# Kernel tuning notes

Measured on AMD Instinct MI355X. Metric: run time of the kernel, lower is better.

## Reference

```python
import jax, jax.numpy as jnp
import numpy as np

B, N, DIN, DOUT = 32, 1024, 256, 256


def setup_inputs() -> dict:
    key = jax.random.key(0)
    ks = jax.random.split(key, 7)
    s = 1.0 / np.sqrt(DIN)
    return {
        "x": jax.random.normal(ks[0], (B, N, DIN), dtype=jnp.float32),
        "Wq": jax.random.uniform(ks[1], (DOUT, DIN), minval=-s, maxval=s, dtype=jnp.float32),
        "bq": jax.random.uniform(ks[2], (DOUT,), minval=-s, maxval=s, dtype=jnp.float32),
        "Wk": jax.random.uniform(ks[3], (DOUT, DIN), minval=-s, maxval=s, dtype=jnp.float32),
        "bk": jax.random.uniform(ks[4], (DOUT,), minval=-s, maxval=s, dtype=jnp.float32),
        "Wv": jax.random.uniform(ks[5], (DOUT, DIN), minval=-s, maxval=s, dtype=jnp.float32),
        "bv": jax.random.uniform(ks[6], (DOUT,), minval=-s, maxval=s, dtype=jnp.float32),
    }


def reference(x, Wq, bq, Wk, bk, Wv, bv):
    # q, k, v: (B, N, Dout)
    q = jnp.einsum("bnd,od->bno", x, Wq) + bq
    k = jnp.einsum("bnd,od->bno", x, Wk) + bk
    v = jnp.einsum("bnd,od->bno", x, Wv) + bv
    # logits: (B, N, N) = q @ k^T per batch
    logits = jnp.einsum("bnd,bmd->bnm", q, k)
    # NOTE: softmax over the BATCH dim (axis=0), as in the original module
    attn = jax.nn.softmax(logits, axis=0)
    out = jnp.einsum("bnm,bmd->bnd", attn, v)  # (B, N, Dout)
    return out
```

## Files before the change

### kernel.cpp

```cpp
#include <hip/hip_runtime.h>

typedef __bf16 bf16x8 __attribute__((ext_vector_type(8)));
typedef __bf16 bf16x4 __attribute__((ext_vector_type(4)));
typedef float  f32x4  __attribute__((ext_vector_type(4)));

#define BK 64

__device__ __forceinline__ void g2l16(const void* g, void* l) {
    __builtin_amdgcn_global_load_lds((const __attribute__((address_space(1))) void*)g,
                                     (__attribute__((address_space(3))) void*)l, 16, 0, 0);
}


__global__ __launch_bounds__(256)
void gemm_proj(const __bf16* __restrict__ A, const __bf16* __restrict__ Wb,
               __bf16* __restrict__ qkv, const float* __restrict__ bpack)
{
    __shared__ __align__(16) __bf16 smem[3 * 12288];

    const int tid  = threadIdx.x;
    const int w    = tid >> 6;
    const int lane = tid & 63;
    const int quad = lane >> 4;
    const int l16  = lane & 15;
    const int wm   = w & 1;
    const int wn   = w >> 1;

    const int m0 = blockIdx.x * 128;
    const int n0 = blockIdx.y * 64;
    const int z  = blockIdx.z;

    const __bf16* Bb   = Wb + (size_t)z * 131072;
    const float*  bias = bpack + z * 256;

    const int srow = (w << 3) + (lane >> 3);
    const int scol = ((lane & 7) ^ (lane >> 3)) << 3;

    const __bf16* Ag = A  + (size_t)(m0 + srow) * 256 + scol;
    const __bf16* Bg = Bb + (size_t)(n0 + srow) * 256 + scol;

    f32x4 acc[4][2] = {};

    auto STAGE = [&](int buf, int k0) {
        char* base = (char*)smem + buf * 24576;
        #pragma unroll
        for (int c = 0; c < 4; c++)
            g2l16(Ag + (size_t)(c * 32) * 256 + k0, base + w * 1024 + c * 4096);
        #pragma unroll
        for (int c = 0; c < 2; c++)
            g2l16(Bg + (size_t)(c * 32) * 256 + k0, base + 16384 + w * 1024 + c * 4096);
    };

    STAGE(0, 0);
    STAGE(1, 64);

    for (int t = 0; t < 4; t++) {
        if (t < 3) asm volatile("s_waitcnt vmcnt(6)" ::: "memory");
        else       asm volatile("s_waitcnt vmcnt(0)" ::: "memory");
        __builtin_amdgcn_sched_barrier(0);
        __builtin_amdgcn_s_barrier();

        if (t < 2) STAGE((t + 2) % 3, (t + 2) * BK);

        const __bf16* As = smem + (t % 3) * 12288;
        const __bf16* Bs = As + 8192;
        #pragma unroll
        for (int kk = 0; kk < BK; kk += 32) {
            const int ub = kk >> 3;
            bf16x8 a[4], b[2];
            #pragma unroll
            for (int mt = 0; mt < 4; mt++) {
                const int row = wm * 64 + mt * 16 + l16;
                const int cp  = ((quad + ub) ^ (row & 7)) << 3;
                a[mt] = *(const bf16x8*)&As[row * BK + cp];
            }
            #pragma unroll
            for (int nt = 0; nt < 2; nt++) {
                const int row = wn * 32 + nt * 16 + l16;
                const int cp  = ((quad + ub) ^ (row & 7)) << 3;
                b[nt] = *(const bf16x8*)&Bs[row * BK + cp];
            }
            #pragma unroll
            for (int mt = 0; mt < 4; mt++)
                #pragma unroll
                for (int nt = 0; nt < 2; nt++)
                    acc[mt][nt] = __builtin_amdgcn_mfma_f32_16x16x32_bf16(
                        a[mt], b[nt], acc[mt][nt], 0, 0, 0);
        }
    }

    __syncthreads();
    if (z < 2) {
        #pragma unroll
        for (int mt = 0; mt < 4; mt++) {
            const int rl = wm * 64 + mt * 16 + quad * 4;
            #pragma unroll
            for (int nt = 0; nt < 2; nt++) {
                const int cl = wn * 32 + nt * 16 + l16;
                const float bn = bias[n0 + cl];
                #pragma unroll
                for (int r = 0; r < 4; r++) {
                    const int row = rl + r;
                    smem[row * 64 + ((((cl >> 3) ^ (row & 7)) << 3) | (cl & 7))] =
                        (__bf16)(acc[mt][nt][r] + bn);
                }
            }
        }
        __syncthreads();
        __bf16* C = qkv + (size_t)z * 8388608;
        #pragma unroll
        for (int i = 0; i < 4; i++) {
            const int c   = tid + i * 256;
            const int row = c >> 3, u = c & 7;
            *(bf16x8*)&C[(size_t)(m0 + row) * 256 + n0 + u * 8] =
                *(const bf16x8*)&smem[row * 64 + ((u ^ (row & 7)) << 3)];
        }
    } else {
        #pragma unroll
        for (int mt = 0; mt < 4; mt++) {
            const int ml = wm * 64 + mt * 16 + quad * 4;
            #pragma unroll
            for (int nt = 0; nt < 2; nt++) {
                const int dl = wn * 32 + nt * 16 + l16;
                const float bn = bias[n0 + dl];
                bf16x4 pk;
                #pragma unroll
                for (int r = 0; r < 4; r++) pk[r] = (__bf16)(acc[mt][nt][r] + bn);
                *(bf16x4*)&smem[dl * 128 + ((((ml >> 3) ^ (dl & 7)) << 3) | (ml & 7))] = pk;
            }
        }
        __syncthreads();
        __bf16* C = qkv + 2 * 8388608;
        const int bidx = m0 >> 10, mbase = m0 & 1023;
        #pragma unroll
        for (int i = 0; i < 4; i++) {
            const int c  = tid + i * 256;
            const int dl = c >> 4, u = c & 15;
            *(bf16x8*)&C[(size_t)bidx * 262144 + (size_t)(n0 + dl) * 1024 + mbase + u * 8] =
                *(const bf16x8*)&smem[dl * 128 + ((u ^ (dl & 7)) << 3)];
        }
    }
}

__global__ __launch_bounds__(256, 1)
void gemm_logits(const __bf16* __restrict__ Q, const __bf16* __restrict__ Km,
                 __bf16* __restrict__ E)
{
    __shared__ __align__(16) __bf16 smem[2 * 24576];

    const int tid  = threadIdx.x;
    const int w    = tid >> 6;
    const int lane = tid & 63;
    const int quad = lane >> 4;
    const int l16  = lane & 15;
    const int wm   = w & 1;
    const int wn   = w >> 1;

    const int id = blockIdx.x;
    const int x  = id & 7, g = id >> 3;
    const int z  = x + ((g >> 5) << 3);
    const int gt = g & 31;
    const int m0 = (gt & 7) * 128;
    const int n0 = (gt >> 3) * 256;

    const __bf16* Ab = Q  + (size_t)z * 262144;
    const __bf16* Bb = Km + (size_t)z * 262144;

    const int srow = (w << 3) + (lane >> 3);
    const int scol = ((lane & 7) ^ (lane >> 3)) << 3;

    const __bf16* Ag = Ab + (size_t)(m0 + srow) * 256 + scol;
    const __bf16* Bg = Bb + (size_t)(n0 + srow) * 256 + scol;

    f32x4 acc[4][8] = {};

    auto STAGE = [&](int buf, int k0) {
        char* base = (char*)smem + buf * 49152;
        #pragma unroll
        for (int c = 0; c < 4; c++)
            g2l16(Ag + (size_t)(c * 32) * 256 + k0, base + w * 1024 + c * 4096);
        #pragma unroll
        for (int c = 0; c < 8; c++)
            g2l16(Bg + (size_t)(c * 32) * 256 + k0, base + 16384 + w * 1024 + c * 4096);
    };

    STAGE(0, 0);
    STAGE(1, 64);

    for (int t = 0; t < 4; t++) {
        if (t < 3) asm volatile("s_waitcnt vmcnt(12)" ::: "memory");
        else       asm volatile("s_waitcnt vmcnt(0)"  ::: "memory");
        __builtin_amdgcn_sched_barrier(0);
        __builtin_amdgcn_s_barrier();

        const __bf16* As = smem + (t & 1) * 24576;
        const __bf16* Bs = As + 8192;
        #pragma unroll
        for (int kk = 0; kk < BK; kk += 32) {
            const int ub = kk >> 3;
            bf16x8 a[4], b[8];
            #pragma unroll
            for (int mt = 0; mt < 4; mt++) {
                const int row = wm * 64 + mt * 16 + l16;
                const int cp  = ((quad + ub) ^ (row & 7)) << 3;
                a[mt] = *(const bf16x8*)&As[row * BK + cp];
            }
            #pragma unroll
            for (int nt = 0; nt < 8; nt++) {
                const int row = wn * 128 + nt * 16 + l16;
                const int cp  = ((quad + ub) ^ (row & 7)) << 3;
                b[nt] = *(const bf16x8*)&Bs[row * BK + cp];
            }
            #pragma unroll
            for (int mt = 0; mt < 4; mt++)
                #pragma unroll
                for (int nt = 0; nt < 8; nt++)
                    acc[mt][nt] = __builtin_amdgcn_mfma_f32_16x16x32_bf16(
                        a[mt], b[nt], acc[mt][nt], 0, 0, 0);
        }

        __builtin_amdgcn_s_barrier();

        if (t < 2) STAGE(t & 1, (t + 2) * BK);
    }

    __syncthreads();
    #pragma unroll
    for (int mt = 0; mt < 4; mt++) {
        const int rl = wm * 64 + mt * 16 + quad * 4;
        #pragma unroll
        for (int nt = 0; nt < 8; nt++) {
            const int cl = wn * 128 + nt * 16 + l16;
            #pragma unroll
            for (int r = 0; r < 4; r++) {
                const int row = rl + r;
                smem[row * 256 + ((((cl >> 3) ^ (row & 7)) << 3) | (cl & 7))] =
                    (__bf16)__expf(acc[mt][nt][r]);
            }
        }
    }
    __syncthreads();
    __bf16* C = E + (size_t)z * 1048576;
    #pragma unroll
    for (int i = 0; i < 16; i++) {
        const int c   = tid + i * 256;
        const int row = c >> 5, u = c & 31;
        *(bf16x8*)&C[(size_t)(m0 + row) * 1024 + n0 + u * 8] =
            *(const bf16x8*)&smem[row * 256 + ((u ^ (row & 7)) << 3)];
    }
}

__global__ __launch_bounds__(256)
void sum_rcp(const __bf16* __restrict__ E, __bf16* __restrict__ rcpS)
{
    const size_t p = (size_t)blockIdx.x * 256 + threadIdx.x;
    const bf16x8* E8 = (const bf16x8*)E;
    float s[8] = {0.f, 0.f, 0.f, 0.f, 0.f, 0.f, 0.f, 0.f};
    #pragma unroll
    for (int b = 0; b < 32; b++) {
        const bf16x8 e = E8[(size_t)b * 131072 + p];
        #pragma unroll
        for (int j = 0; j < 8; j++) s[j] += (float)e[j];
    }
    bf16x8 o;
    #pragma unroll
    for (int j = 0; j < 8; j++) o[j] = (__bf16)__builtin_amdgcn_rcpf(s[j]);
    ((bf16x8*)rcpS)[p] = o;
}

__global__ __launch_bounds__(256, 1)
void gemm_pv(const __bf16* __restrict__ En, const __bf16* __restrict__ rcpS,
             const __bf16* __restrict__ vT, float* __restrict__ out)
{
    __shared__ __align__(16) __bf16 smem[2 * 24576];

    const int tid  = threadIdx.x;
    const int w    = tid >> 6;
    const int lane = tid & 63;
    const int quad = lane >> 4;
    const int l16  = lane & 15;
    const int wm   = w & 1;
    const int wn   = w >> 1;

    const int id = blockIdx.x;
    const int x  = id & 7, g = id >> 3;
    const int z  = x + ((g & 3) << 3);
    const int m0 = (g >> 2) * 128;

    const __bf16* Eb = En + (size_t)z * 1048576;
    const __bf16* Vb = vT + (size_t)z * 262144;
    float*        Ob = out + (size_t)z * 262144;

    const int srow = (w << 3) + (lane >> 3);
    const int scol = ((lane & 7) ^ (lane >> 3)) << 3;

    const __bf16* Ag = Eb   + (size_t)(m0 + srow) * 1024 + scol;
    const __bf16* Rg = rcpS + (size_t)(m0 + srow) * 1024 + scol;
    const __bf16* Bg = Vb   + (size_t)srow * 1024 + scol;

    f32x4 acc[4][8] = {};
    bf16x8 e[4], rs[4];

    auto LOAD_ER = [&](int k0) {
        #pragma unroll
        for (int c = 0; c < 4; c++) {
            e[c]  = *(const bf16x8*)(Ag + (size_t)(c * 32) * 1024 + k0);
            rs[c] = *(const bf16x8*)(Rg + (size_t)(c * 32) * 1024 + k0);
        }
    };
    auto G2L_B = [&](int buf, int k0) {
        char* base = (char*)smem + buf * 49152 + 16384;
        #pragma unroll
        for (int c = 0; c < 8; c++)
            g2l16(Bg + (size_t)(c * 32) * 1024 + k0, base + w * 1024 + c * 4096);
    };
    auto WRITE_A = [&](int buf) {
        char* base = (char*)smem + buf * 49152;
        #pragma unroll
        for (int c = 0; c < 4; c++) {
            bf16x8 o;
            #pragma unroll
            for (int j = 0; j < 8; j++)
                o[j] = (__bf16)((float)e[c][j] * (float)rs[c][j]);
            *(bf16x8*)(base + w * 1024 + lane * 16 + c * 4096) = o;
        }
    };

    LOAD_ER(0);
    G2L_B(0, 0);
    asm volatile("s_waitcnt vmcnt(8)" ::: "memory");
    __builtin_amdgcn_sched_barrier(0);
    WRITE_A(0);
    LOAD_ER(64);
    G2L_B(1, 64);

    for (int t = 0; t < 16; t++) {
        if (t < 15) asm volatile("s_waitcnt vmcnt(16)" ::: "memory");
        else        asm volatile("s_waitcnt vmcnt(0)"  ::: "memory");
        __builtin_amdgcn_sched_barrier(0);
        asm volatile("s_waitcnt lgkmcnt(0)" ::: "memory");
        __builtin_amdgcn_sched_barrier(0);
        __builtin_amdgcn_s_barrier();

        const __bf16* As = smem + (t & 1) * 24576;
        const __bf16* Bs = As + 8192;
        #pragma unroll
        for (int kk = 0; kk < BK; kk += 32) {
            const int ub = kk >> 3;
            bf16x8 a[4], b[8];
            #pragma unroll
            for (int mt = 0; mt < 4; mt++) {
                const int row = wm * 64 + mt * 16 + l16;
                const int cp  = ((quad + ub) ^ (row & 7)) << 3;
                a[mt] = *(const bf16x8*)&As[row * BK + cp];
            }
            #pragma unroll
            for (int nt = 0; nt < 8; nt++) {
                const int row = wn * 128 + nt * 16 + l16;
                const int cp  = ((quad + ub) ^ (row & 7)) << 3;
                b[nt] = *(const bf16x8*)&Bs[row * BK + cp];
            }
            #pragma unroll
            for (int mt = 0; mt < 4; mt++)
                #pragma unroll
                for (int nt = 0; nt < 8; nt++)
                    acc[mt][nt] = __builtin_amdgcn_mfma_f32_16x16x32_bf16(
                        a[mt], b[nt], acc[mt][nt], 0, 0, 0);
        }

        __builtin_amdgcn_s_barrier();

        if (t < 15) {
            asm volatile("s_waitcnt vmcnt(8)" ::: "memory");
            __builtin_amdgcn_sched_barrier(0);
            WRITE_A((t + 1) & 1);
            if (t < 14) {
                LOAD_ER((t + 2) * BK);
                G2L_B(t & 1, (t + 2) * BK);
            }
        }
    }

    #pragma unroll
    for (int mt = 0; mt < 4; mt++) {
        const int mb = m0 + wm * 64 + mt * 16 + quad * 4;
        #pragma unroll
        for (int nt = 0; nt < 8; nt++) {
            const int n = wn * 128 + nt * 16 + l16;
            #pragma unroll
            for (int r = 0; r < 4; r++)
                Ob[(size_t)(mb + r) * 256 + n] = acc[mt][nt][r];
        }
    }
}

__global__ __launch_bounds__(256)
void cvt_all(const float* __restrict__ x,
             const float* __restrict__ Wq, const float* __restrict__ Wk,
             const float* __restrict__ Wv,
             const float* __restrict__ bq, const float* __restrict__ bk,
             const float* __restrict__ bv,
             __bf16* __restrict__ xb, __bf16* __restrict__ Wqb,
             float* __restrict__ bpack)
{
    const int i = blockIdx.x * 256 + threadIdx.x;
    if (i < 1073152) {
        const float* s; __bf16* d; int off;
        if (i < 1048576)      { s = x;  d = xb;            off = i; }
        else if (i < 1056768) { s = Wq; d = Wqb;           off = i - 1048576; }
        else if (i < 1064960) { s = Wk; d = Wqb + 131072;  off = i - 1056768; }
        else                  { s = Wv; d = Wqb + 262144;  off = i - 1064960; }
        const float4* s4 = (const float4*)s;
        const float4 f0 = s4[off * 2], f1 = s4[off * 2 + 1];
        bf16x8 o;
        o[0] = (__bf16)f0.x; o[1] = (__bf16)f0.y; o[2] = (__bf16)f0.z; o[3] = (__bf16)f0.w;
        o[4] = (__bf16)f1.x; o[5] = (__bf16)f1.y; o[6] = (__bf16)f1.z; o[7] = (__bf16)f1.w;
        ((bf16x8*)d)[off] = o;
    } else if (i < 1073344) {
        const int j = i - 1073152;
        const int sel = j >> 6, jj = j & 63;
        const float* s = sel == 0 ? bq : (sel == 1 ? bk : bv);
        ((float4*)bpack)[j] = ((const float4*)s)[jj];
    }
}

extern "C" void kernel_launch(void* const* d_in, const int* in_sizes, int n_in,
                              void* d_out, int out_size, void* d_ws, size_t ws_size,
                              hipStream_t stream)
{
    const float* x  = (const float*)d_in[0];
    const float* Wq = (const float*)d_in[1];
    const float* bq = (const float*)d_in[2];
    const float* Wk = (const float*)d_in[3];
    const float* bk = (const float*)d_in[4];
    const float* Wv = (const float*)d_in[5];
    const float* bv = (const float*)d_in[6];
    float* out = (float*)d_out;

    char* ws = (char*)d_ws;
    __bf16* rcpS = (__bf16*)ws;
    __bf16* xb   = (__bf16*)(ws + (2u  << 20));
    __bf16* qkv  = (__bf16*)(ws + (18u << 20));
    __bf16* E    = (__bf16*)(ws + (66u << 20));
    __bf16* Wqb  = (__bf16*)(ws + (130u << 20));
    float*  bpack = (float*)(ws + (130u << 20) + (1u << 20));

    cvt_all<<<4194, 256, 0, stream>>>(x, Wq, Wk, Wv, bq, bk, bv, xb, Wqb, bpack);

    gemm_proj<<<dim3(256, 4, 3), 256, 0, stream>>>(xb, Wqb, qkv, bpack);

    gemm_logits<<<1024, 256, 0, stream>>>(qkv, qkv + 8388608, E);

    sum_rcp<<<512, 256, 0, stream>>>(E, rcpS);

    gemm_pv<<<256, 256, 0, stream>>>(E, rcpS, qkv + 2 * 8388608, out);
}
```

Before: 188.6 us.

## Make gemm_logits blocks persistent over full rows with register-resident Q fragments

Each gemm_logits block now owns a 128-row Q strip and walks all four 256-column K tiles, instead of one 128x256 output tile per block. The Q strip is loaded into LDS once and held in registers across tiles, while K tiles are streamed through a double buffer that keeps prefetching during each tile's exp/store epilogue. The grid shrinks from 1024 to 256 blocks, one per CU, which removes repeated Q loads and the block tail across waves. The cost is heavy register pressure from the resident A fragments plus accumulators, 128KB of LDS, and less parallelism to hide latency.

```diff
diff --git a/kernel.cpp b/kernel.cpp
--- a/kernel.cpp
+++ b/kernel.cpp
@@ -146,7 +146,7 @@
 void gemm_logits(const __bf16* __restrict__ Q, const __bf16* __restrict__ Km,
                  __bf16* __restrict__ E)
 {
-    __shared__ __align__(16) __bf16 smem[2 * 24576];
+    __shared__ __align__(16) __bf16 smem[65536];
 
     const int tid  = threadIdx.x;
     const int w    = tid >> 6;
@@ -158,10 +158,8 @@
 
     const int id = blockIdx.x;
     const int x  = id & 7, g = id >> 3;
-    const int z  = x + ((g >> 5) << 3);
-    const int gt = g & 31;
-    const int m0 = (gt & 7) * 128;
-    const int n0 = (gt >> 3) * 256;
+    const int z  = x + ((g & 3) << 3);
+    const int m0 = (g >> 2) * 128;
 
     const __bf16* Ab = Q  + (size_t)z * 262144;
     const __bf16* Bb = Km + (size_t)z * 262144;
@@ -170,83 +168,112 @@
     const int scol = ((lane & 7) ^ (lane >> 3)) << 3;
 
     const __bf16* Ag = Ab + (size_t)(m0 + srow) * 256 + scol;
-    const __bf16* Bg = Bb + (size_t)(n0 + srow) * 256 + scol;
-
-    f32x4 acc[4][8] = {};
-
-    auto STAGE = [&](int buf, int k0) {
-        char* base = (char*)smem + buf * 49152;
+    const __bf16* Bg = Bb + (size_t)srow * 256 + scol;
+
+    #pragma unroll
+    for (int kc = 0; kc < 4; kc++)
         #pragma unroll
         for (int c = 0; c < 4; c++)
-            g2l16(Ag + (size_t)(c * 32) * 256 + k0, base + w * 1024 + c * 4096);
+            g2l16(Ag + (size_t)(c * 32) * 256 + kc * 64,
+                  (char*)smem + kc * 16384 + w * 1024 + c * 4096);
+
+    auto STAGE_B = [&](int buf, int tile, int k0) {
+        char* base = (char*)smem + 65536 + buf * 32768;
         #pragma unroll
         for (int c = 0; c < 8; c++)
-            g2l16(Bg + (size_t)(c * 32) * 256 + k0, base + 16384 + w * 1024 + c * 4096);
+            g2l16(Bg + (size_t)(tile * 256 + c * 32) * 256 + k0,
+                  base + w * 1024 + c * 4096);
     };
-
-    STAGE(0, 0);
-    STAGE(1, 64);
-
-    for (int t = 0; t < 4; t++) {
-        if (t < 3) asm volatile("s_waitcnt vmcnt(12)" ::: "memory");
-        else       asm volatile("s_waitcnt vmcnt(0)"  ::: "memory");
+    STAGE_B(0, 0, 0);
+    STAGE_B(1, 0, 64);
+
+    asm volatile("s_waitcnt vmcnt(16)" ::: "memory");
+    __builtin_amdgcn_sched_barrier(0);
+    __builtin_amdgcn_s_barrier();
+
+    bf16x8 afr[4][8];
+    #pragma unroll
+    for (int mt = 0; mt < 4; mt++) {
+        const int row = wm * 64 + mt * 16 + l16;
+        #pragma unroll
+        for (int kc = 0; kc < 4; kc++)
+            #pragma unroll
+            for (int h = 0; h < 2; h++)
+                afr[mt][kc * 2 + h] =
+                    *(const bf16x8*)&smem[kc * 8192 + row * 64 +
+                                          ((((quad + h * 4)) ^ (row & 7)) << 3)];
+    }
+
+    f32x4 acc[4][8];
+    __bf16* C = E + (size_t)z * 1048576;
+
+    #pragma unroll
+    for (int tile = 0; tile < 4; tile++) {
+        #pragma unroll
+        for (int mt = 0; mt < 4; mt++)
+            #pragma unroll
+            for (int nt = 0; nt < 8; nt++)
+                acc[mt][nt] = f32x4{0.f, 0.f, 0.f, 0.f};
+
+        #pragma unroll
+        for (int j = 0; j < 4; j++) {
+            const int i = tile * 4 + j;
+            if (tile == 0)          asm volatile("s_waitcnt vmcnt(8)"  ::: "memory");
+            else if (j < 2)         asm volatile("s_waitcnt vmcnt(24)" ::: "memory");
+            else if (i == 15)       asm volatile("s_waitcnt vmcnt(0)"  ::: "memory");
+            else                    asm volatile("s_waitcnt vmcnt(8)"  ::: "memory");
+            __builtin_amdgcn_sched_barrier(0);
+            __builtin_amdgcn_s_barrier();
+
+            const __bf16* Bs = smem + 32768 + (i & 1) * 16384;
+            #pragma unroll
+            for (int h = 0; h < 2; h++) {
+                bf16x8 b[8];
+                #pragma unroll
+                for (int nt = 0; nt < 8; nt++) {
+                    const int row = wn * 128 + nt * 16 + l16;
+                    const int cp  = ((quad + h * 4) ^ (row & 7)) << 3;
+                    b[nt] = *(const bf16x8*)&Bs[row * BK + cp];
+                }
+                #pragma unroll
+                for (int mt = 0; mt < 4; mt++)
+                    #pragma unroll
+                    for (int nt = 0; nt < 8; nt++)
+                        acc[mt][nt] = __builtin_amdgcn_mfma_f32_16x16x32_bf16(
+                            afr[mt][j * 2 + h], b[nt], acc[mt][nt], 0, 0, 0);
+            }
+            __builtin_amdgcn_s_barrier();
+
+            if (i + 2 <= 15)
+                STAGE_B(i & 1, (i + 2) >> 2, ((i + 2) & 3) * 64);
+        }
+
+        #pragma unroll
+        for (int mt = 0; mt < 4; mt++) {
+            const int rl = wm * 64 + mt * 16 + quad * 4;
+            #pragma unroll
+            for (int nt = 0; nt < 8; nt++) {
+                const int cl = wn * 128 + nt * 16 + l16;
+                #pragma unroll
+                for (int r = 0; r < 4; r++) {
+                    const int row = rl + r;
+                    smem[row * 256 + ((((cl >> 3) ^ (row & 7)) << 3) | (cl & 7))] =
+                        (__bf16)__expf(acc[mt][nt][r]);
+                }
+            }
+        }
+        asm volatile("s_waitcnt lgkmcnt(0)" ::: "memory");
         __builtin_amdgcn_sched_barrier(0);
         __builtin_amdgcn_s_barrier();
 
-        const __bf16* As = smem + (t & 1) * 24576;
-        const __bf16* Bs = As + 8192;
-        #pragma unroll
-        for (int kk = 0; kk < BK; kk += 32) {
-            const int ub = kk >> 3;
-            bf16x8 a[4], b[8];
-            #pragma unroll
-            for (int mt = 0; mt < 4; mt++) {
-                const int row = wm * 64 + mt * 16 + l16;
-                const int cp  = ((quad + ub) ^ (row & 7)) << 3;
-                a[mt] = *(const bf16x8*)&As[row * BK + cp];
-            }
-            #pragma unroll
-            for (int nt = 0; nt < 8; nt++) {
-                const int row = wn * 128 + nt * 16 + l16;
-                const int cp  = ((quad + ub) ^ (row & 7)) << 3;
-                b[nt] = *(const bf16x8*)&Bs[row * BK + cp];
-            }
-            #pragma unroll
-            for (int mt = 0; mt < 4; mt++)
-                #pragma unroll
-                for (int nt = 0; nt < 8; nt++)
-                    acc[mt][nt] = __builtin_amdgcn_mfma_f32_16x16x32_bf16(
-                        a[mt], b[nt], acc[mt][nt], 0, 0, 0);
-        }
-
-        __builtin_amdgcn_s_barrier();
-
-        if (t < 2) STAGE(t & 1, (t + 2) * BK);
-    }
-
-    __syncthreads();
-    #pragma unroll
-    for (int mt = 0; mt < 4; mt++) {
-        const int rl = wm * 64 + mt * 16 + quad * 4;
-        #pragma unroll
-        for (int nt = 0; nt < 8; nt++) {
-            const int cl = wn * 128 + nt * 16 + l16;
-            #pragma unroll
-            for (int r = 0; r < 4; r++) {
-                const int row = rl + r;
-                smem[row * 256 + ((((cl >> 3) ^ (row & 7)) << 3) | (cl & 7))] =
-                    (__bf16)__expf(acc[mt][nt][r]);
-            }
-        }
-    }
-    __syncthreads();
-    __bf16* C = E + (size_t)z * 1048576;
-    #pragma unroll
-    for (int i = 0; i < 16; i++) {
-        const int c   = tid + i * 256;
-        const int row = c >> 5, u = c & 31;
-        *(bf16x8*)&C[(size_t)(m0 + row) * 1024 + n0 + u * 8] =
-            *(const bf16x8*)&smem[row * 256 + ((u ^ (row & 7)) << 3)];
+        const int n0 = tile * 256;
+        #pragma unroll
+        for (int ii = 0; ii < 16; ii++) {
+            const int c   = tid + ii * 256;
+            const int row = c >> 5, u = c & 31;
+            *(bf16x8*)&C[(size_t)(m0 + row) * 1024 + n0 + u * 8] =
+                *(const bf16x8*)&smem[row * 256 + ((u ^ (row & 7)) << 3)];
+        }
     }
 }
 
@@ -449,7 +476,7 @@
 
     gemm_proj<<<dim3(256, 4, 3), 256, 0, stream>>>(xb, Wqb, qkv, bpack);
 
-    gemm_logits<<<1024, 256, 0, stream>>>(qkv, qkv + 8388608, E);
+    gemm_logits<<<256, 256, 0, stream>>>(qkv, qkv + 8388608, E);
 
     sum_rcp<<<512, 256, 0, stream>>>(E, rcpS);
 
```

Result: slower. 200.6 us (+6.4%).
